# Optimization experiments

Hardware: AMD Instinct MI355X
Metric: run time of the kernel (lower is better)

The kernel has to match this reference:

```python
import jax, jax.numpy as jnp
import numpy as np

B, BUFF, STK, NCOMP, HIST = 128, 64, 48, 8, 96
VOCAB, WDIM, POSN, POSD = 100000, 300, 50, 50
DEP, CAD, HAD, FC, U = 40, 50, 50, 128, 256
NOUT = 2 + 2 * DEP


def setup_inputs() -> dict:
    key = jax.random.key(0)
    ks = jax.random.split(key, 40)
    d = {}
    d['buff_word_id'] = jax.random.randint(ks[0], (B, BUFF), 0, VOCAB)
    d['buff_pos_id'] = jax.random.randint(ks[1], (B, BUFF), 0, POSN)
    d['comp_word_id'] = jax.random.randint(ks[2], (B, STK, 2 * NCOMP), 0, VOCAB)
    d['comp_pos_id'] = jax.random.randint(ks[3], (B, STK, 2 * NCOMP), 0, POSN)
    d['comp_action_id'] = jax.random.randint(ks[4], (B, STK, NCOMP), 0, 2 * DEP)
    d['comp_action_len'] = jax.random.randint(ks[5], (B, STK), 0, NCOMP + 1)
    d['history_action_id'] = jax.random.randint(ks[6], (B, HIST), 0, 3 + 4 * DEP)
    d['stack_length'] = jax.random.randint(ks[7], (B,), 1, STK + 1)
    d['buff_length'] = jax.random.randint(ks[8], (B,), 1, BUFF + 1)
    d['history_action_length'] = jax.random.randint(ks[9], (B,), 1, HIST + 1)

    def w(k, shape):
        return jax.random.normal(k, shape, jnp.float32) / np.sqrt(shape[0])

    d['p_emb'] = jax.random.normal(ks[10], (POSN, POSD), jnp.float32) * 0.1
    d['comp_a_emb'] = jax.random.normal(ks[11], (2 * DEP, CAD), jnp.float32) * 0.1
    d['hist_a_emb'] = jax.random.normal(ks[12], (3 + 4 * DEP, HAD), jnp.float32) * 0.1
    d['w_emb'] = jax.random.normal(ks[13], (VOCAB, WDIM), jnp.float32) * 0.1
    d['emb_W'] = w(ks[14], (WDIM + POSD, FC)); d['emb_b'] = jnp.zeros((FC,), jnp.float32)
    d['rec_W'] = w(ks[15], (FC + CAD + FC, FC)); d['rec_b'] = jnp.zeros((FC,), jnp.float32)
    d['sW0'] = w(ks[16], (FC + U, 4 * U)); d['sb0'] = jnp.zeros((4 * U,), jnp.float32)
    d['sW1'] = w(ks[17], (U + U, 4 * U)); d['sb1'] = jnp.zeros((4 * U,), jnp.float32)
    d['bW0'] = w(ks[18], (FC + U, 4 * U)); d['bb0'] = jnp.zeros((4 * U,), jnp.float32)
    d['bW1'] = w(ks[19], (U + U, 4 * U)); d['bb1'] = jnp.zeros((4 * U,), jnp.float32)
    d['aW0'] = w(ks[20], (HAD + U, 4 * U)); d['ab0'] = jnp.zeros((4 * U,), jnp.float32)
    d['aW1'] = w(ks[21], (U + U, 4 * U)); d['ab1'] = jnp.zeros((4 * U,), jnp.float32)
    d['fW'] = w(ks[22], (3 * U, NOUT)); d['fb'] = jnp.zeros((NOUT,), jnp.float32)
    return d


def _lstm_cell(c, h, x, W, b):
    # TF LSTMCell gate order: i, j (candidate), f, o; forget_bias = 1.0
    z = jnp.concatenate([x, h], -1) @ W + b
    i, j, f, o = jnp.split(z, 4, -1)
    c = c * jax.nn.sigmoid(f + 1.0) + jax.nn.sigmoid(i) * jnp.tanh(j)
    h = jnp.tanh(c) * jax.nn.sigmoid(o)
    return c, h


def _run_lstm2(x, lengths, W0, b0, W1, b1):
    # x: [B, T, D]; returns final (at t = length) second-layer h, like dynamic_rnn's state[1].h
    Bb, T, _ = x.shape
    u = W0.shape[1] // 4
    init = tuple(jnp.zeros((Bb, u), x.dtype) for _ in range(4))

    def step(carry, inp):
        xt, t = inp
        c0, h0, c1, h1 = carry
        nc0, nh0 = _lstm_cell(c0, h0, xt, W0, b0)
        nc1, nh1 = _lstm_cell(c1, h1, nh0, W1, b1)
        m = (t < lengths)[:, None]
        new = tuple(jnp.where(m, n, o) for n, o in zip((nc0, nh0, nc1, nh1), carry))
        return new, None

    (c0, h0, c1, h1), _ = jax.lax.scan(step, init, (x.transpose(1, 0, 2), jnp.arange(T)))
    return h1


def _compose(word_id, comp_emb, act_emb, a_len, rec_W, rec_b):
    # word_id: [2N] int, comp_emb: [2N, FC], act_emb: [N, CAD], a_len: scalar
    # Sequential dict-keyed recursive composition (dict keys are head word ids).
    N = act_emb.shape[0]
    head_ids = word_id[0::2]
    dep_ids = word_id[1::2]
    idxs = jnp.arange(N)

    def step(vals, n):
        mask_h = (head_ids == head_ids[n]) & (idxs < n)
        mask_d = (head_ids == dep_ids[n]) & (idxs < n)
        ih = jnp.max(jnp.where(mask_h, idxs, -1))
        idd = jnp.max(jnp.where(mask_d, idxs, -1))
        head_e = jnp.where(ih >= 0, vals[jnp.maximum(ih, 0)], comp_emb[2 * n])
        dep_e = jnp.where(idd >= 0, vals[jnp.maximum(idd, 0)], comp_emb[2 * n + 1])
        new = jnp.tanh(jnp.concatenate([head_e, act_emb[n], dep_e]) @ rec_W + rec_b)
        return vals.at[n].set(new), new

    vals0 = jnp.zeros((N, rec_W.shape[1]), comp_emb.dtype)
    _, news = jax.lax.scan(step, vals0, idxs)
    return jnp.where(a_len == 0, comp_emb[0], news[jnp.maximum(a_len - 1, 0)])


def reference(buff_word_id, buff_pos_id, comp_word_id, comp_pos_id, comp_action_id,
              comp_action_len, history_action_id, stack_length, buff_length,
              history_action_length, p_emb, comp_a_emb, hist_a_emb, w_emb,
              emb_W, emb_b, rec_W, rec_b, sW0, sb0, sW1, sb1, bW0, bb0, bW1, bb1,
              aW0, ab0, aW1, ab1, fW, fb):
    buff_emb = jax.nn.relu(
        jnp.concatenate([w_emb[buff_word_id], p_emb[buff_pos_id]], -1) @ emb_W + emb_b)
    comp_emb = jax.nn.relu(
        jnp.concatenate([w_emb[comp_word_id], p_emb[comp_pos_id]], -1) @ emb_W + emb_b)
    act_emb = comp_a_emb[comp_action_id]        # [B, STK, N, CAD]
    hist_emb = hist_a_emb[history_action_id]    # [B, HIST, HAD]

    comp_fn = lambda wi, ce, ae, al: _compose(wi, ce, ae, al, rec_W, rec_b)
    stack_emb = jax.vmap(jax.vmap(comp_fn))(comp_word_id, comp_emb, act_emb, comp_action_len)

    h_s = _run_lstm2(stack_emb, stack_length, sW0, sb0, sW1, sb1)
    h_b = _run_lstm2(buff_emb, buff_length, bW0, bb0, bW1, bb1)
    h_a = _run_lstm2(hist_emb, history_action_length, aW0, ab0, aW1, ab1)
    return jnp.concatenate([h_s, h_b, h_a], -1) @ fW + fb
```

## Files before the change

kernel.cpp:

```cpp
#include <hip/hip_runtime.h>

#define BB    128
#define BUFF  64
#define STK   48
#define NCOMP 8
#define HIST  96
#define WDIM  300
#define POSD  50
#define CAD   50
#define HAD   50
#define FC    128
#define UU    256
#define NOUT  82

typedef __bf16 bf16;
typedef __attribute__((ext_vector_type(8))) __bf16 bf16x8;
typedef __attribute__((ext_vector_type(4))) float   f32x4;

__device__ __forceinline__ float sigf(float x)   { return 1.f / (1.f + __expf(-x)); }
__device__ __forceinline__ float tanhf_(float x) { return 1.f - 2.f / (1.f + __expf(2.f * x)); }

__device__ __forceinline__ unsigned pack2(const float* p) {
  union { unsigned u; bf16 h[2]; } r;
  r.h[0] = (bf16)p[0]; r.h[1] = (bf16)p[1];
  return r.u;
}

__device__ __forceinline__ bf16x8 aload16(const bf16* p) {
  union { unsigned long long q[2]; bf16x8 v; } u;
  u.q[0] = __hip_atomic_load((const unsigned long long*)p,       __ATOMIC_RELAXED, __HIP_MEMORY_SCOPE_AGENT);
  u.q[1] = __hip_atomic_load((const unsigned long long*)(p + 4), __ATOMIC_RELAXED, __HIP_MEMORY_SCOPE_AGENT);
  return u.v;
}

__global__ __launch_bounds__(256) void k_emb(
    const int* bw, const int* bp, const int* cw, const int* cp,
    const float* w_emb, const float* p_emb, const float* embW, const float* embB,
    bf16* comp_emb, bf16* buff_emb)
{
  __shared__ __align__(16) char sm[138752];
  bf16*  A  = (bf16*)sm;
  bf16*  Wt = (bf16*)(sm + 46080);
  float* sb = (float*)(sm + 46080 + 92160);

  const int tid = threadIdx.x;
  const int r0  = blockIdx.x * 64;

  for (int i = tid; i < 64 * 176; i += 256) {
    int m = i / 176, c2 = i % 176, e0 = 2 * c2;
    int r = r0 + m;
    unsigned v;
    if (e0 < 300) {
      int word = (r < 98304) ? cw[r] : bw[r - 98304];
      v = pack2(w_emb + word * 300 + e0);
    } else if (e0 < 350) {
      int pos = (r < 98304) ? cp[r] : bp[r - 98304];
      v = pack2(p_emb + pos * 50 + (e0 - 300));
    } else v = 0u;
    *(unsigned*)(A + m * 360 + e0) = v;
  }
  for (int i = tid; i < 350 * 128; i += 256) {
    int k = i >> 7, n = i & 127;
    Wt[n * 360 + k] = (bf16)embW[i];
  }
  { int i = tid; if (i < 256) { int n = i >> 1; Wt[n * 360 + 350 + (i & 1)] = (bf16)0.f; } }
  if (tid < 128) sb[tid] = embB[tid];
  __syncthreads();

  const int wv = tid >> 6, lane = tid & 63, l15 = lane & 15, quad = lane >> 4;
  f32x4 acc[8];
#pragma unroll
  for (int i = 0; i < 8; ++i) acc[i] = (f32x4){0.f, 0.f, 0.f, 0.f};

  const bf16* Arow = A + (wv * 16 + l15) * 360;
  for (int ks = 0; ks < 11; ++ks) {
    int kq = ks * 32 + quad * 8;
    bf16x8 a = *(const bf16x8*)(Arow + kq);
#pragma unroll
    for (int nt = 0; nt < 8; ++nt) {
      bf16x8 b = *(const bf16x8*)(Wt + (nt * 16 + l15) * 360 + kq);
      acc[nt] = __builtin_amdgcn_mfma_f32_16x16x32_bf16(a, b, acc[nt], 0, 0, 0);
    }
  }
#pragma unroll
  for (int nt = 0; nt < 8; ++nt)
#pragma unroll
    for (int rr = 0; rr < 4; ++rr) {
      int row = wv * 16 + quad * 4 + rr;
      int n   = nt * 16 + l15;
      float z = fmaxf(acc[nt][rr] + sb[n], 0.f);
      int r = r0 + row;
      bf16 o = (bf16)z;
      if (r < 98304) comp_emb[r * 128 + n] = o;
      else           buff_emb[(r - 98304) * 128 + n] = o;
    }
}

__global__ __launch_bounds__(256) void k_compose(
    const int* cw, const int* caid, const int* calen,
    const bf16* comp_emb, const float* ca_emb, const float* recW, const float* recB,
    bf16* stack_emb)
{
  __shared__ __align__(16) char sm[129344];
  bf16*  Wt   = (bf16*)sm;
  bf16*  X    = (bf16*)(sm + 83968);
  bf16*  VALS = (bf16*)(sm + 94464);
  float* recb = (float*)(sm + 127232);
  int*   IH   = (int*)(sm + 127744);
  int*   ID   = (int*)(sm + 128256);
  int*   AN   = (int*)(sm + 128768);
  int*   ALEN = (int*)(sm + 129280);

  const int tid = threadIdx.x;
  const int bs0 = blockIdx.x * 16;

  for (int i = tid; i < 306 * 128; i += 256) {
    int k = i >> 7, n = i & 127;
    Wt[n * 328 + k] = (bf16)recW[i];
  }
  for (int i = tid; i < 128 * 22; i += 256) {
    int n = i / 22, k = 306 + i % 22;
    Wt[n * 328 + k] = (bf16)0.f;
  }
  if (tid < 128) recb[tid] = recB[tid];
  if (tid < 16) {
    int bs = bs0 + tid;
    int hid[8], did[8];
#pragma unroll
    for (int m = 0; m < 8; ++m) { hid[m] = cw[bs * 16 + 2 * m]; did[m] = cw[bs * 16 + 2 * m + 1]; }
    for (int n = 0; n < 8; ++n) {
      int ih = -1, idd = -1;
      for (int m = 0; m < n; ++m) { if (hid[m] == hid[n]) ih = m; if (hid[m] == did[n]) idd = m; }
      IH[tid * 8 + n] = ih; ID[tid * 8 + n] = idd; AN[tid * 8 + n] = caid[bs * 8 + n];
    }
    ALEN[tid] = calen[bs];
  }
  __syncthreads();

  const int wv = tid >> 6, lane = tid & 63, l15 = lane & 15, quad = lane >> 4;

  for (int n = 0; n < 8; ++n) {
    for (int i = tid; i < 16 * 160; i += 256) {
      int p = i / 160, c2 = i % 160, e0 = 2 * c2;
      int bs = bs0 + p;
      unsigned v;
      if (e0 < 128) {
        int ih = IH[p * 8 + n];
        v = (ih >= 0) ? *(const unsigned*)(VALS + (p * 8 + ih) * 128 + e0)
                      : *(const unsigned*)(comp_emb + (bs * 16 + 2 * n) * 128 + e0);
      } else if (e0 < 178) {
        v = pack2(ca_emb + AN[p * 8 + n] * 50 + (e0 - 128));
      } else if (e0 < 306) {
        int e = e0 - 178;
        int idd = ID[p * 8 + n];
        v = (idd >= 0) ? *(const unsigned*)(VALS + (p * 8 + idd) * 128 + e)
                       : *(const unsigned*)(comp_emb + (bs * 16 + 2 * n + 1) * 128 + e);
      } else v = 0u;
      *(unsigned*)(X + p * 328 + e0) = v;
    }
    __syncthreads();

    f32x4 acc[2];
    acc[0] = (f32x4){0.f,0.f,0.f,0.f}; acc[1] = (f32x4){0.f,0.f,0.f,0.f};
    for (int ks = 0; ks < 10; ++ks) {
      int kq = ks * 32 + quad * 8;
      bf16x8 a = *(const bf16x8*)(X + l15 * 328 + kq);
#pragma unroll
      for (int t2 = 0; t2 < 2; ++t2) {
        int nt = 2 * wv + t2;
        bf16x8 b = *(const bf16x8*)(Wt + (nt * 16 + l15) * 328 + kq);
        acc[t2] = __builtin_amdgcn_mfma_f32_16x16x32_bf16(a, b, acc[t2], 0, 0, 0);
      }
    }
    __syncthreads();
#pragma unroll
    for (int t2 = 0; t2 < 2; ++t2) {
      int nt = 2 * wv + t2;
#pragma unroll
      for (int rr = 0; rr < 4; ++rr) {
        int p = quad * 4 + rr;
        int col = nt * 16 + l15;
        VALS[(p * 8 + n) * 128 + col] = (bf16)tanhf_(acc[t2][rr] + recb[col]);
      }
    }
    __syncthreads();
  }

  for (int i = tid; i < 16 * 64; i += 256) {
    int p = i / 64, c2 = i % 64, e0 = 2 * c2;
    int bs = bs0 + p;
    int al = ALEN[p];
    unsigned v = (al == 0) ? *(const unsigned*)(comp_emb + (bs * 16) * 128 + e0)
                           : *(const unsigned*)(VALS + (p * 8 + (al - 1)) * 128 + e0);
    *(unsigned*)(stack_emb + bs * 128 + e0) = v;
  }
}

struct BarT { int cnt; int pad[31]; };

__global__ __launch_bounds__(256) void k_lstm(
    const float* sW0, const float* sb0, const float* sW1, const float* sb1,
    const float* bW0, const float* bb0, const float* bW1, const float* bb1,
    const float* aW0, const float* ab0, const float* aW1, const float* ab1,
    const bf16* stack_emb, const bf16* buff_emb, const float* hist_tab, const int* hist_id,
    const int* len_s, const int* len_b, const int* len_a,
    bf16* h0buf, bf16* h1buf, BarT* bars)
{
  __shared__ __align__(16) char sm[143872];
  const int tid = threadIdx.x;
  const int bx  = blockIdx.x;
  const int L     = bx >> 4;
  const int rid   = bx & 15;
  const int layer = rid >> 3;
  const int u0    = (rid & 7) * 32;
  const int T     = (L == 0) ? STK : (L == 1) ? BUFF : HIST;
  const int* lenp = (L == 0) ? len_s : (L == 1) ? len_b : len_a;

  const float *W, *bias;
  int K, KP, Kxp;
  if (layer == 0) {
    W = (L == 0) ? sW0 : (L == 1) ? bW0 : aW0;
    bias = (L == 0) ? sb0 : (L == 1) ? bb0 : ab0;
    if (L == 2) { K = 320; KP = 328; Kxp = 64; } else { K = 384; KP = 392; Kxp = 128; }
  } else {
    W = (L == 0) ? sW1 : (L == 1) ? bW1 : aW1;
    bias = (L == 0) ? sb1 : (L == 1) ? bb1 : ab1;
    K = 512; KP = 520; Kxp = 256;
  }
  bf16*  Wt     = (bf16*)sm;
  bf16*  hstage = (bf16*)(sm + 128 * KP * 2);
  float* sb     = (float*)(sm + 128 * KP * 2 + 9216);
  bf16*  Xa     = (bf16*)(sm + 128 * KP * 2 + 9216 + 512);

  for (int i = tid; i < K * 128; i += 256) {
    int kk = i >> 7, cc = i & 127;
    int col = (cc >> 5) * 256 + u0 + (cc & 31);
    bf16 v;
    if (layer == 0 && L == 2) {
      if (kk < 64) v = (kk < 50) ? (bf16)W[kk * 1024 + col] : (bf16)0.f;
      else         v = (bf16)W[(kk - 14) * 1024 + col];
    } else v = (bf16)W[kk * 1024 + col];
    Wt[cc * KP + kk] = v;
  }
  if (tid < 128) { int col = (tid >> 5) * 256 + u0 + (tid & 31); sb[tid] = bias[col]; }

  const int wv = tid >> 6, lane = tid & 63, l15 = lane & 15, quad = lane >> 4;
  int lenr[8];
#pragma unroll
  for (int mt = 0; mt < 2; ++mt)
#pragma unroll
    for (int rr = 0; rr < 4; ++rr)
      lenr[mt * 4 + rr] = lenp[32 * wv + 16 * mt + quad * 4 + rr];

  float cst[16], hst[16];
#pragma unroll
  for (int i = 0; i < 16; ++i) { cst[i] = 0.f; hst[i] = 0.f; }

  BarT* bar = bars + L;
  bf16* h0w = h0buf + L * 2 * 32768;
  bf16* h1w = h1buf + L * 2 * 32768;
  const bf16* xsrc = (L == 0) ? stack_emb : buff_emb;
  const int Tx = (L == 0) ? STK : BUFF;

  __syncthreads();

  for (int p = 0; p <= T; ++p) {
    const bool active = (layer == 0) ? (p < T) : (p >= 1);
    const int  t = (layer == 0) ? p : (p - 1);

    if (L == 2 && layer == 0 && active) {
      for (int i = tid; i < 128 * 32; i += 256) {
        int row = i >> 5, e0 = 2 * (i & 31);
        unsigned v = 0u;
        if (e0 < 50) { int id = hist_id[row * 96 + t]; v = pack2(hist_tab + id * 50 + e0); }
        *(unsigned*)(Xa + row * 72 + e0) = v;
      }
    }
    __syncthreads();

    if (active) {
      f32x4 acc[2][8];
#pragma unroll
      for (int a1 = 0; a1 < 2; ++a1)
#pragma unroll
        for (int a2 = 0; a2 < 8; ++a2) acc[a1][a2] = (f32x4){0.f, 0.f, 0.f, 0.f};

      const bf16* h0r = h0w + ((p - 1) & 1) * 32768;
      const bf16* h1r = h1w + (p & 1) * 32768;

      for (int ks = 0; ks < K / 32; ++ks) {
        int k0 = ks * 32;
        int kq = k0 + quad * 8;
        bf16x8 a[2];
#pragma unroll
        for (int mt = 0; mt < 2; ++mt) {
          int row = 32 * wv + 16 * mt + l15;
          if (layer == 0) {
            if (k0 < Kxp) {
              if (L == 2) a[mt] = *(const bf16x8*)(Xa + row * 72 + kq);
              else        a[mt] = *(const bf16x8*)(xsrc + (row * Tx + t) * 128 + kq);
            } else a[mt] = aload16(h0r + row * 256 + (kq - Kxp));
          } else {
            if (k0 < 256) a[mt] = aload16(h0r + row * 256 + kq);
            else          a[mt] = aload16(h1r + row * 256 + (kq - 256));
          }
        }
#pragma unroll
        for (int nt = 0; nt < 8; ++nt) {
          bf16x8 b = *(const bf16x8*)(Wt + (nt * 16 + l15) * KP + kq);
          acc[0][nt] = __builtin_amdgcn_mfma_f32_16x16x32_bf16(a[0], b, acc[0][nt], 0, 0, 0);
          acc[1][nt] = __builtin_amdgcn_mfma_f32_16x16x32_bf16(a[1], b, acc[1][nt], 0, 0, 0);
        }
      }
#pragma unroll
      for (int mt = 0; mt < 2; ++mt)
#pragma unroll
        for (int g2 = 0; g2 < 2; ++g2)
#pragma unroll
          for (int rr = 0; rr < 4; ++rr) {
            int row = 32 * wv + 16 * mt + quad * 4 + rr;
            float zi = acc[mt][0 + g2][rr] + sb[(0 + g2) * 16 + l15];
            float zj = acc[mt][2 + g2][rr] + sb[(2 + g2) * 16 + l15];
            float zf = acc[mt][4 + g2][rr] + sb[(4 + g2) * 16 + l15];
            float zo = acc[mt][6 + g2][rr] + sb[(6 + g2) * 16 + l15];
            float ig = sigf(zi), jg = tanhf_(zj), fg = sigf(zf + 1.f), og = sigf(zo);
            int idx = mt * 8 + g2 * 4 + rr;
            float cn = cst[idx] * fg + ig * jg;
            float hn = tanhf_(cn) * og;
            bool mk = (t < lenr[mt * 4 + rr]);
            cst[idx] = mk ? cn : cst[idx];
            hst[idx] = mk ? hn : hst[idx];
            hstage[row * 36 + g2 * 16 + l15] = (bf16)hst[idx];
          }
    }
    __syncthreads();
    if (active) {
      bf16* dst = (layer == 0) ? (h0w + (p & 1) * 32768) : (h1w + ((p - 1) & 1) * 32768);
      for (int i = tid; i < 128 * 8; i += 256) {
        int row = i >> 3, c = i & 7;
        unsigned long long v = *(const unsigned long long*)(hstage + row * 36 + c * 4);
        __hip_atomic_store((unsigned long long*)(dst + row * 256 + u0 + c * 4), v,
                           __ATOMIC_RELAXED, __HIP_MEMORY_SCOPE_AGENT);
      }
    }
    __syncthreads();
    if (tid == 0) {
      __builtin_amdgcn_sched_barrier(0);
      const int target = 16 * (p + 1);
      int prev = __hip_atomic_fetch_add(&bar->cnt, 1, __ATOMIC_RELAXED, __HIP_MEMORY_SCOPE_AGENT);
      if (prev != target - 1) {
        while (__hip_atomic_load(&bar->cnt, __ATOMIC_RELAXED, __HIP_MEMORY_SCOPE_AGENT) < target) { }
      }
      __builtin_amdgcn_sched_barrier(0);
    }
    __syncthreads();
  }
}

__global__ __launch_bounds__(128) void k_final(
    const bf16* h1buf, const float* fW, const float* fb, float* out)
{
  __shared__ float hs[768];
  const int b = blockIdx.x, tid = threadIdx.x;
  for (int i = tid; i < 768; i += 128) {
    int L = i >> 8, u = i & 255;
    hs[i] = (float)h1buf[(L * 2 + 1) * 32768 + b * 256 + u];
  }
  __syncthreads();
  if (tid < NOUT) {
    float acc = fb[tid];
    for (int u = 0; u < 768; ++u) acc += hs[u] * fW[u * NOUT + tid];
    out[b * NOUT + tid] = acc;
  }
}

extern "C" void kernel_launch(void* const* d_in, const int* in_sizes, int n_in,
                              void* d_out, int out_size, void* d_ws, size_t ws_size,
                              hipStream_t stream)
{
  (void)in_sizes; (void)n_in; (void)out_size; (void)ws_size;
  char* ws = (char*)d_ws;
  BarT* bars      = (BarT*)ws;
  bf16* h0buf     = (bf16*)(ws + 512);
  bf16* h1buf     = (bf16*)(ws + 512 + 393216);
  bf16* comp_emb  = (bf16*)(ws + 786944);
  bf16* buff_emb  = (bf16*)(ws + 786944 + 25165824);
  bf16* stack_emb = (bf16*)(ws + 786944 + 25165824 + 2097152);

  hipMemsetAsync(ws, 0, 786944, stream);

  k_emb<<<1664, 256, 0, stream>>>(
      (const int*)d_in[0], (const int*)d_in[1], (const int*)d_in[2], (const int*)d_in[3],
      (const float*)d_in[13], (const float*)d_in[10], (const float*)d_in[14], (const float*)d_in[15],
      comp_emb, buff_emb);

  k_compose<<<384, 256, 0, stream>>>(
      (const int*)d_in[2], (const int*)d_in[4], (const int*)d_in[5],
      comp_emb, (const float*)d_in[11], (const float*)d_in[16], (const float*)d_in[17],
      stack_emb);

  k_lstm<<<48, 256, 0, stream>>>(
      (const float*)d_in[18], (const float*)d_in[19], (const float*)d_in[20], (const float*)d_in[21],
      (const float*)d_in[22], (const float*)d_in[23], (const float*)d_in[24], (const float*)d_in[25],
      (const float*)d_in[26], (const float*)d_in[27], (const float*)d_in[28], (const float*)d_in[29],
      stack_emb, buff_emb, (const float*)d_in[12], (const int*)d_in[6],
      (const int*)d_in[7], (const int*)d_in[8], (const int*)d_in[9],
      h0buf, h1buf, bars);

  k_final<<<128, 128, 0, stream>>>(h1buf, (const float*)d_in[30], (const float*)d_in[31],
                                   (float*)d_out);
}
```

Before: 2.115 ms.

## Template LSTM roles and prefetch recurrent state before input-projection MFMAs

```diff
diff --git a/kernel.cpp b/kernel.cpp
--- a/kernel.cpp
+++ b/kernel.cpp
@@ -24,13 +24,6 @@
   union { unsigned u; bf16 h[2]; } r;
   r.h[0] = (bf16)p[0]; r.h[1] = (bf16)p[1];
   return r.u;
-}
-
-__device__ __forceinline__ bf16x8 aload16(const bf16* p) {
-  union { unsigned long long q[2]; bf16x8 v; } u;
-  u.q[0] = __hip_atomic_load((const unsigned long long*)p,       __ATOMIC_RELAXED, __HIP_MEMORY_SCOPE_AGENT);
-  u.q[1] = __hip_atomic_load((const unsigned long long*)(p + 4), __ATOMIC_RELAXED, __HIP_MEMORY_SCOPE_AGENT);
-  return u.v;
 }
 
 __global__ __launch_bounds__(256) void k_emb(
@@ -198,35 +191,19 @@
 
 struct BarT { int cnt; int pad[31]; };
 
-__global__ __launch_bounds__(256) void k_lstm(
-    const float* sW0, const float* sb0, const float* sW1, const float* sb1,
-    const float* bW0, const float* bb0, const float* bW1, const float* bb1,
-    const float* aW0, const float* ab0, const float* aW1, const float* ab1,
-    const bf16* stack_emb, const bf16* buff_emb, const float* hist_tab, const int* hist_id,
-    const int* len_s, const int* len_b, const int* len_a,
-    bf16* h0buf, bf16* h1buf, BarT* bars)
-{
-  __shared__ __align__(16) char sm[143872];
+template<int L, int LAYER>
+__device__ __forceinline__ void lstm_role(
+    const float* W, const float* bias,
+    const bf16* xsrc, const float* hist_tab, const int* hist_id,
+    const int* lenp, bf16* h0w, bf16* h1w, BarT* bar, char* sm, int u0)
+{
+  constexpr int T   = (L == 0) ? STK : (L == 1) ? BUFF : HIST;
+  constexpr int K   = (LAYER == 0) ? ((L == 2) ? 320 : 384) : 512;
+  constexpr int KP  = K + 8;
+  constexpr int Kxp = (LAYER == 0) ? ((L == 2) ? 64 : 128) : 256;
+  constexpr int Tx  = (L == 0) ? STK : BUFF;
+
   const int tid = threadIdx.x;
-  const int bx  = blockIdx.x;
-  const int L     = bx >> 4;
-  const int rid   = bx & 15;
-  const int layer = rid >> 3;
-  const int u0    = (rid & 7) * 32;
-  const int T     = (L == 0) ? STK : (L == 1) ? BUFF : HIST;
-  const int* lenp = (L == 0) ? len_s : (L == 1) ? len_b : len_a;
-
-  const float *W, *bias;
-  int K, KP, Kxp;
-  if (layer == 0) {
-    W = (L == 0) ? sW0 : (L == 1) ? bW0 : aW0;
-    bias = (L == 0) ? sb0 : (L == 1) ? bb0 : ab0;
-    if (L == 2) { K = 320; KP = 328; Kxp = 64; } else { K = 384; KP = 392; Kxp = 128; }
-  } else {
-    W = (L == 0) ? sW1 : (L == 1) ? bW1 : aW1;
-    bias = (L == 0) ? sb1 : (L == 1) ? bb1 : ab1;
-    K = 512; KP = 520; Kxp = 256;
-  }
   bf16*  Wt     = (bf16*)sm;
   bf16*  hstage = (bf16*)(sm + 128 * KP * 2);
   float* sb     = (float*)(sm + 128 * KP * 2 + 9216);
@@ -236,7 +213,7 @@
     int kk = i >> 7, cc = i & 127;
     int col = (cc >> 5) * 256 + u0 + (cc & 31);
     bf16 v;
-    if (layer == 0 && L == 2) {
+    if (LAYER == 0 && L == 2) {
       if (kk < 64) v = (kk < 50) ? (bf16)W[kk * 1024 + col] : (bf16)0.f;
       else         v = (bf16)W[(kk - 14) * 1024 + col];
     } else v = (bf16)W[kk * 1024 + col];
@@ -256,19 +233,15 @@
 #pragma unroll
   for (int i = 0; i < 16; ++i) { cst[i] = 0.f; hst[i] = 0.f; }
 
-  BarT* bar = bars + L;
-  bf16* h0w = h0buf + L * 2 * 32768;
-  bf16* h1w = h1buf + L * 2 * 32768;
-  const bf16* xsrc = (L == 0) ? stack_emb : buff_emb;
-  const int Tx = (L == 0) ? STK : BUFF;
+  const int row0 = 32 * wv + l15;
 
   __syncthreads();
 
   for (int p = 0; p <= T; ++p) {
-    const bool active = (layer == 0) ? (p < T) : (p >= 1);
-    const int  t = (layer == 0) ? p : (p - 1);
-
-    if (L == 2 && layer == 0 && active) {
+    const bool active = (LAYER == 0) ? (p < T) : (p >= 1);
+    const int  t = (LAYER == 0) ? p : (p - 1);
+
+    if (L == 2 && LAYER == 0 && active) {
       for (int i = tid; i < 128 * 32; i += 256) {
         int row = i >> 5, e0 = 2 * (i & 31);
         unsigned v = 0u;
@@ -279,39 +252,83 @@
     __syncthreads();
 
     if (active) {
-      f32x4 acc[2][8];
-#pragma unroll
-      for (int a1 = 0; a1 < 2; ++a1)
-#pragma unroll
-        for (int a2 = 0; a2 < 8; ++a2) acc[a1][a2] = (f32x4){0.f, 0.f, 0.f, 0.f};
-
       const bf16* h0r = h0w + ((p - 1) & 1) * 32768;
       const bf16* h1r = h1w + (p & 1) * 32768;
 
-      for (int ks = 0; ks < K / 32; ++ks) {
-        int k0 = ks * 32;
-        int kq = k0 + quad * 8;
-        bf16x8 a[2];
+      bf16x8 hA[16];
+#pragma unroll
+      for (int hk = 0; hk < 8; ++hk)
 #pragma unroll
         for (int mt = 0; mt < 2; ++mt) {
-          int row = 32 * wv + 16 * mt + l15;
-          if (layer == 0) {
-            if (k0 < Kxp) {
-              if (L == 2) a[mt] = *(const bf16x8*)(Xa + row * 72 + kq);
-              else        a[mt] = *(const bf16x8*)(xsrc + (row * Tx + t) * 128 + kq);
-            } else a[mt] = aload16(h0r + row * 256 + (kq - Kxp));
-          } else {
-            if (k0 < 256) a[mt] = aload16(h0r + row * 256 + kq);
-            else          a[mt] = aload16(h1r + row * 256 + (kq - 256));
+          const bf16* pa = h0r + (row0 + 16 * mt) * 256 + hk * 32 + quad * 8;
+          asm volatile("global_load_dwordx4 %0, %1, off sc0 sc1"
+                       : "=v"(hA[hk * 2 + mt]) : "v"(pa) : "memory");
+        }
+      bf16x8 hB[16];
+      if (LAYER == 1) {
+#pragma unroll
+        for (int hk = 0; hk < 8; ++hk)
+#pragma unroll
+          for (int mt = 0; mt < 2; ++mt) {
+            const bf16* pb = h1r + (row0 + 16 * mt) * 256 + hk * 32 + quad * 8;
+            asm volatile("global_load_dwordx4 %0, %1, off sc0 sc1"
+                         : "=v"(hB[hk * 2 + mt]) : "v"(pb) : "memory");
+          }
+      }
+
+      f32x4 acc[2][8];
+#pragma unroll
+      for (int a1 = 0; a1 < 2; ++a1)
+#pragma unroll
+        for (int a2 = 0; a2 < 8; ++a2) acc[a1][a2] = (f32x4){0.f, 0.f, 0.f, 0.f};
+
+      if (LAYER == 0) {
+#pragma unroll
+        for (int ks = 0; ks < Kxp / 32; ++ks) {
+          int kq = ks * 32 + quad * 8;
+          bf16x8 a[2];
+#pragma unroll
+          for (int mt = 0; mt < 2; ++mt) {
+            int row = row0 + 16 * mt;
+            if (L == 2) a[mt] = *(const bf16x8*)(Xa + row * 72 + kq);
+            else        a[mt] = *(const bf16x8*)(xsrc + (row * Tx + t) * 128 + kq);
+          }
+#pragma unroll
+          for (int nt = 0; nt < 8; ++nt) {
+            bf16x8 b = *(const bf16x8*)(Wt + (nt * 16 + l15) * KP + kq);
+            acc[0][nt] = __builtin_amdgcn_mfma_f32_16x16x32_bf16(a[0], b, acc[0][nt], 0, 0, 0);
+            acc[1][nt] = __builtin_amdgcn_mfma_f32_16x16x32_bf16(a[1], b, acc[1][nt], 0, 0, 0);
           }
         }
+      }
+
+      asm volatile("s_waitcnt vmcnt(0)" ::: "memory");
+      __builtin_amdgcn_sched_barrier(0);
+
+      constexpr int HB0 = (LAYER == 0) ? Kxp : 0;
+#pragma unroll
+      for (int hk = 0; hk < 8; ++hk) {
+        int kq = HB0 + hk * 32 + quad * 8;
 #pragma unroll
         for (int nt = 0; nt < 8; ++nt) {
           bf16x8 b = *(const bf16x8*)(Wt + (nt * 16 + l15) * KP + kq);
-          acc[0][nt] = __builtin_amdgcn_mfma_f32_16x16x32_bf16(a[0], b, acc[0][nt], 0, 0, 0);
-          acc[1][nt] = __builtin_amdgcn_mfma_f32_16x16x32_bf16(a[1], b, acc[1][nt], 0, 0, 0);
+          acc[0][nt] = __builtin_amdgcn_mfma_f32_16x16x32_bf16(hA[hk * 2 + 0], b, acc[0][nt], 0, 0, 0);
+          acc[1][nt] = __builtin_amdgcn_mfma_f32_16x16x32_bf16(hA[hk * 2 + 1], b, acc[1][nt], 0, 0, 0);
         }
       }
+      if (LAYER == 1) {
+#pragma unroll
+        for (int hk = 0; hk < 8; ++hk) {
+          int kq = 256 + hk * 32 + quad * 8;
+#pragma unroll
+          for (int nt = 0; nt < 8; ++nt) {
+            bf16x8 b = *(const bf16x8*)(Wt + (nt * 16 + l15) * KP + kq);
+            acc[0][nt] = __builtin_amdgcn_mfma_f32_16x16x32_bf16(hB[hk * 2 + 0], b, acc[0][nt], 0, 0, 0);
+            acc[1][nt] = __builtin_amdgcn_mfma_f32_16x16x32_bf16(hB[hk * 2 + 1], b, acc[1][nt], 0, 0, 0);
+          }
+        }
+      }
+
 #pragma unroll
       for (int mt = 0; mt < 2; ++mt)
 #pragma unroll
@@ -335,7 +352,7 @@
     }
     __syncthreads();
     if (active) {
-      bf16* dst = (layer == 0) ? (h0w + (p & 1) * 32768) : (h1w + ((p - 1) & 1) * 32768);
+      bf16* dst = (LAYER == 0) ? (h0w + (p & 1) * 32768) : (h1w + ((p - 1) & 1) * 32768);
       for (int i = tid; i < 128 * 8; i += 256) {
         int row = i >> 3, c = i & 7;
         unsigned long long v = *(const unsigned long long*)(hstage + row * 36 + c * 4);
@@ -343,17 +360,50 @@
                            __ATOMIC_RELAXED, __HIP_MEMORY_SCOPE_AGENT);
       }
     }
-    __syncthreads();
-    if (tid == 0) {
-      __builtin_amdgcn_sched_barrier(0);
-      const int target = 16 * (p + 1);
-      int prev = __hip_atomic_fetch_add(&bar->cnt, 1, __ATOMIC_RELAXED, __HIP_MEMORY_SCOPE_AGENT);
-      if (prev != target - 1) {
-        while (__hip_atomic_load(&bar->cnt, __ATOMIC_RELAXED, __HIP_MEMORY_SCOPE_AGENT) < target) { }
-      }
-      __builtin_amdgcn_sched_barrier(0);
-    }
-    __syncthreads();
+    if (p < T) {
+      __syncthreads();
+      if (tid == 0) {
+        __builtin_amdgcn_sched_barrier(0);
+        const int target = 16 * (p + 1);
+        int prev = __hip_atomic_fetch_add(&bar->cnt, 1, __ATOMIC_RELAXED, __HIP_MEMORY_SCOPE_AGENT);
+        if (prev != target - 1) {
+          while (__hip_atomic_load(&bar->cnt, __ATOMIC_RELAXED, __HIP_MEMORY_SCOPE_AGENT) < target) { }
+        }
+        __builtin_amdgcn_sched_barrier(0);
+      }
+      __syncthreads();
+    }
+  }
+}
+
+__global__ __launch_bounds__(256, 1) void k_lstm(
+    const float* sW0, const float* sb0, const float* sW1, const float* sb1,
+    const float* bW0, const float* bb0, const float* bW1, const float* bb1,
+    const float* aW0, const float* ab0, const float* aW1, const float* ab1,
+    const bf16* stack_emb, const bf16* buff_emb, const float* hist_tab, const int* hist_id,
+    const int* len_s, const int* len_b, const int* len_a,
+    bf16* h0buf, bf16* h1buf, BarT* bars)
+{
+  __shared__ __align__(16) char sm[143872];
+  const int bx    = blockIdx.x;
+  const int L     = bx >> 4;
+  const int rid   = bx & 15;
+  const int layer = rid >> 3;
+  const int u0    = (rid & 7) * 32;
+
+  BarT* bar = bars + L;
+  bf16* h0w = h0buf + L * 2 * 32768;
+  bf16* h1w = h1buf + L * 2 * 32768;
+
+  if (L == 0) {
+    if (layer == 0) lstm_role<0, 0>(sW0, sb0, stack_emb, hist_tab, hist_id, len_s, h0w, h1w, bar, sm, u0);
+    else            lstm_role<0, 1>(sW1, sb1, stack_emb, hist_tab, hist_id, len_s, h0w, h1w, bar, sm, u0);
+  } else if (L == 1) {
+    if (layer == 0) lstm_role<1, 0>(bW0, bb0, buff_emb, hist_tab, hist_id, len_b, h0w, h1w, bar, sm, u0);
+    else            lstm_role<1, 1>(bW1, bb1, buff_emb, hist_tab, hist_id, len_b, h0w, h1w, bar, sm, u0);
+  } else {
+    if (layer == 0) lstm_role<2, 0>(aW0, ab0, nullptr, hist_tab, hist_id, len_a, h0w, h1w, bar, sm, u0);
+    else            lstm_role<2, 1>(aW1, ab1, nullptr, hist_tab, hist_id, len_a, h0w, h1w, bar, sm, u0);
   }
 }
 
```

Measured after the change: 1.944 ms. 1.09x faster.
